# Kernel tuning notes

Hardware: AMD Instinct MI355X
Metric: run time of the kernel (lower is better)

The kernel has to match this reference:

```python
import jax, jax.numpy as jnp
import numpy as np

# model dims
D = 2048      # hidden_size
H = 16        # num_attention_heads
KV = 4        # num_key_value_heads
DH = 128      # head_dim
RD = 64       # rotary_dim (partial RoPE)
E = 8         # num_local_experts
TOPK = 2      # num_experts_per_tok
I = 1024      # intermediate_size
EPS = 1e-6
THETA = 1000000.0


def rmsnorm(h, w, eps=EPS):
    dt = h.dtype
    h32 = h.astype(jnp.float32)
    var = jnp.mean(h32 * h32, axis=-1, keepdims=True)
    return (w * (h32 * jax.lax.rsqrt(var + eps))).astype(dt)


def rotate_half(t):
    half = t.shape[-1] // 2
    return jnp.concatenate([-t[..., half:], t[..., :half]], axis=-1)


def setup_inputs() -> dict:
    key = jax.random.key(0)
    ks = jax.random.split(key, 16)
    s = lambda k, shape, sc: (jax.random.normal(k, shape, dtype=jnp.float32) * sc)
    B, S = 1, 2048
    return {
        "x": s(ks[0], (B, S, D), 1.0),
        "ln1_w": jnp.ones((D,), jnp.float32),
        "ln2_w": jnp.ones((D,), jnp.float32),
        "wq": s(ks[1], (D, H * DH), 0.02),
        "wk": s(ks[2], (D, KV * DH), 0.02),
        "wv": s(ks[3], (D, KV * DH), 0.02),
        "wo": s(ks[4], (H * DH, D), 0.02),
        "qnorm_w": jnp.ones((H * DH,), jnp.float32),
        "knorm_w": jnp.ones((KV * DH,), jnp.float32),
        "router_w": s(ks[5], (D, E), 0.02),
        "router_bias": s(ks[6], (E,), 0.1),
        "wg": s(ks[7], (E, D, I), 0.02),
        "wu": s(ks[8], (E, D, I), 0.02),
        "wd": s(ks[9], (E, I, D), 0.02),
    }


def reference(x, ln1_w, ln2_w, wq, wk, wv, wo, qnorm_w, knorm_w,
              router_w, router_bias, wg, wu, wd):
    B, S, _ = x.shape
    # ---- input RMSNorm + attention ----
    res = x
    h = rmsnorm(x, ln1_w)
    q = h @ wq                           # [B,S,H*DH]
    k = h @ wk                           # [B,S,KV*DH]
    v = h @ wv
    # MiniMax M2: QK-norm BEFORE reshape, over the full projection dim
    q = rmsnorm(q, qnorm_w)
    k = rmsnorm(k, knorm_w)
    q = q.reshape(B, S, H, DH).transpose(0, 2, 1, 3)    # [B,H,S,DH]
    k = k.reshape(B, S, KV, DH).transpose(0, 2, 1, 3)   # [B,KV,S,DH]
    v = v.reshape(B, S, KV, DH).transpose(0, 2, 1, 3)
    # partial RoPE on first RD dims of each head
    pos = jnp.arange(S, dtype=jnp.float32)
    inv_freq = 1.0 / (THETA ** (jnp.arange(0, RD, 2, dtype=jnp.float32) / RD))
    ang = pos[:, None] * inv_freq[None, :]              # [S,RD/2]
    emb = jnp.concatenate([ang, ang], axis=-1)          # [S,RD]
    cos, sin = jnp.cos(emb), jnp.sin(emb)

    def rope(t):
        rot, pas = t[..., :RD], t[..., RD:]
        rot = rot * cos + rotate_half(rot) * sin
        return jnp.concatenate([rot, pas], axis=-1)

    q, k = rope(q), rope(k)
    # GQA: repeat kv heads
    rep = H // KV
    k = jnp.repeat(k, rep, axis=1)                      # [B,H,S,DH]
    v = jnp.repeat(v, rep, axis=1)
    scores = jnp.einsum("bhqd,bhkd->bhqk", q, k) / np.sqrt(DH)
    causal = jnp.tril(jnp.ones((S, S), dtype=bool))
    scores = jnp.where(causal, scores, jnp.finfo(jnp.float32).min)
    attn = jax.nn.softmax(scores.astype(jnp.float32), axis=-1).astype(q.dtype)
    o = jnp.einsum("bhqk,bhkd->bhqd", attn, v)          # [B,H,S,DH]
    o = o.transpose(0, 2, 1, 3).reshape(B, S, H * DH) @ wo
    x1 = res + o

    # ---- post-attn RMSNorm + sigmoid-router top-k MoE ----
    h2 = rmsnorm(x1, ln2_w)
    t = h2.reshape(-1, D)                               # [T,D]
    T = t.shape[0]
    logits = t.astype(jnp.float32) @ router_w           # router in fp32
    sig = jax.nn.sigmoid(logits)                        # act before topk
    # bias only influences expert choice, not affinities
    _, topi = jax.lax.top_k(sig + router_bias, TOPK)    # [T,TOPK]
    aff = jnp.take_along_axis(sig, topi, axis=-1)
    aff = aff / jnp.sum(aff, axis=-1, keepdims=True)    # normalize_top_k_affinities
    combine = jnp.zeros((T, E), jnp.float32).at[
        jnp.arange(T)[:, None], topi].set(aff)          # [T,E] sparse combine weights
    # GLU expert MLPs (dense over experts; combine zeros out unrouted)
    gate = jnp.einsum("td,edi->tei", t, wg)
    up = jnp.einsum("td,edi->tei", t, wu)
    act = jax.nn.silu(gate) * up                        # [T,E,I]
    moe = jnp.einsum("te,tei,eid->td", combine.astype(t.dtype), act, wd)
    return x1 + moe.reshape(B, S, D)
```

## Files before the change

kernel.cpp:

```cpp
#include <hip/hip_runtime.h>
#include <hip/hip_bf16.h>
#include <stdint.h>
#include <math.h>

typedef __bf16 bf16;
typedef __bf16 bf16x8 __attribute__((ext_vector_type(8)));
typedef __bf16 bf16x4 __attribute__((ext_vector_type(4)));
typedef float  f32x4  __attribute__((ext_vector_type(4)));

#define SD 2048
#define DM 2048
#define NH 16
#define NKV 4
#define DHD 128
#define NE 8
#define NNI 1024

constexpr size_t OF_WQKVT = 0;
constexpr size_t OF_WGUT  = OF_WQKVT + 12582912ull;
constexpr size_t OF_WDT   = OF_WGUT  + 67108864ull;
constexpr size_t OF_WOT   = OF_WDT   + 33554432ull;
constexpr size_t OF_H     = OF_WOT   + 8388608ull;
constexpr size_t OF_QKV   = OF_H     + 8388608ull;
constexpr size_t OF_QB    = OF_QKV   + 25165824ull;
constexpr size_t OF_KB    = OF_QB    + 8388608ull;
constexpr size_t OF_VTB   = OF_KB    + 2097152ull;
constexpr size_t OF_X1    = OF_VTB   + 2097152ull;
constexpr size_t WS_NEED  = OF_X1    + 16777216ull;
constexpr size_t OF_ACT  = OF_QKV;
constexpr size_t OF_TB   = OF_WOT;
constexpr size_t OF_OB   = OF_H;
constexpr size_t OF_CNT  = OF_KB;
constexpr size_t OF_BLKE = OF_KB + 256;
constexpr size_t OF_BLKR = OF_KB + 512;
constexpr size_t OF_TOT  = OF_KB + 768;
constexpr size_t OF_TOPI = OF_KB + 1024;
constexpr size_t OF_TOPW = OF_KB + 16384;
constexpr size_t OF_IDXL = OF_KB + 65536;
constexpr size_t OF_WLST = OF_KB + 131072;
constexpr size_t OF_TMP0 = OF_H;
constexpr size_t OF_TMP1 = OF_WOT;

__device__ __forceinline__ void async16(void* lds, const void* g) {
  uint32_t lo = (uint32_t)(uintptr_t)lds;
  __builtin_amdgcn_global_load_lds(
      (const __attribute__((address_space(1))) uint32_t*)(uintptr_t)g,
      (__attribute__((address_space(3))) uint32_t*)lo,
      16, 0, 0);
}

__global__ void transpose_cvt(const float* __restrict__ in, int ild, long long inb,
                              bf16* __restrict__ out, int old_, long long outb,
                              int ost, int oroff)
{
  __shared__ float tile[32][33];
  const float* ip = in + (long long)blockIdx.z * inb;
  bf16* op = out + (long long)blockIdx.z * outb;
  int r0 = blockIdx.y * 32, c0 = blockIdx.x * 32;
  int tx = threadIdx.x, ty = threadIdx.y;
#pragma unroll
  for (int i = 0; i < 4; i++)
    tile[ty + i*8][tx] = ip[(size_t)(r0 + ty + i*8)*ild + c0 + tx];
  __syncthreads();
#pragma unroll
  for (int i = 0; i < 4; i++) {
    int cl = ty + i*8;
    op[(size_t)((c0 + cl)*ost + oroff)*old_ + r0 + tx] = (bf16)tile[tx][cl];
  }
}

__global__ __launch_bounds__(256)
void rmsnorm_k(const float* __restrict__ in, const float* __restrict__ w, bf16* __restrict__ outb)
{
  __shared__ float red[4];
  int s = blockIdx.x, t = threadIdx.x;
  const float* ip = in + (size_t)s * DM;
  float v[8]; float ss = 0.f;
#pragma unroll
  for (int i = 0; i < 8; i++) { v[i] = ip[t + i*256]; ss += v[i]*v[i]; }
#pragma unroll
  for (int off = 32; off > 0; off >>= 1) ss += __shfl_xor(ss, off);
  if ((t & 63) == 0) red[t >> 6] = ss;
  __syncthreads();
  float rn = rsqrtf((red[0]+red[1]+red[2]+red[3]) * (1.f/DM) + 1e-6f);
  bf16* op = outb + (size_t)s * DM;
#pragma unroll
  for (int i = 0; i < 8; i++) op[t + i*256] = (bf16)(v[i]*rn*w[t + i*256]);
}

__global__ __launch_bounds__(256)
void qrope_k(const float* __restrict__ qkv, const float* __restrict__ w, bf16* __restrict__ qout)
{
  __shared__ float row[2048];
  __shared__ float red[4];
  int s = blockIdx.x, t = threadIdx.x;
  const float* ip = qkv + (size_t)s * 3072;
  float ss = 0.f;
#pragma unroll
  for (int i = 0; i < 8; i++) { float x = ip[t + i*256]; row[t + i*256] = x; ss += x*x; }
#pragma unroll
  for (int off = 32; off > 0; off >>= 1) ss += __shfl_xor(ss, off);
  if ((t & 63) == 0) red[t >> 6] = ss;
  __syncthreads();
  float rn = rsqrtf((red[0]+red[1]+red[2]+red[3]) * (1.f/2048.f) + 1e-6f);
  const float sc = 0.08838834764831845f;
#pragma unroll
  for (int i = 0; i < 8; i++) {
    int idx = t + i*256;
    int d = idx & 127;
    float val = row[idx]*rn*w[idx];
    float o;
    if (d < 64) {
      int fi = d & 31;
      float ang = (float)s * expf(-(float)fi * (13.815510557964274f/32.f));
      float c, sn; sincosf(ang, &sn, &c);
      float pv = row[idx ^ 32]*rn*w[idx ^ 32];
      o = (d < 32) ? (val*c - pv*sn) : (val*c + pv*sn);
    } else o = val;
    qout[((size_t)(idx >> 7)*SD + s)*DHD + d] = (bf16)(o * sc);
  }
}

__global__ __launch_bounds__(128)
void krope_k(const float* __restrict__ qkv, const float* __restrict__ w, bf16* __restrict__ kout)
{
  __shared__ float row[512];
  __shared__ float red[2];
  int s = blockIdx.x, t = threadIdx.x;
  const float* ip = qkv + (size_t)s * 3072 + 2048;
  float ss = 0.f;
#pragma unroll
  for (int i = 0; i < 4; i++) { float x = ip[t + i*128]; row[t + i*128] = x; ss += x*x; }
#pragma unroll
  for (int off = 32; off > 0; off >>= 1) ss += __shfl_xor(ss, off);
  if ((t & 63) == 0) red[t >> 6] = ss;
  __syncthreads();
  float rn = rsqrtf((red[0]+red[1]) * (1.f/512.f) + 1e-6f);
#pragma unroll
  for (int i = 0; i < 4; i++) {
    int idx = t + i*128;
    int d = idx & 127;
    float val = row[idx]*rn*w[idx];
    float o;
    if (d < 64) {
      int fi = d & 31;
      float ang = (float)s * expf(-(float)fi * (13.815510557964274f/32.f));
      float c, sn; sincosf(ang, &sn, &c);
      float pv = row[idx ^ 32]*rn*w[idx ^ 32];
      o = (d < 32) ? (val*c - pv*sn) : (val*c + pv*sn);
    } else o = val;
    kout[((size_t)(idx >> 7)*SD + s)*DHD + d] = (bf16)o;
  }
}

template<int EPI>
__global__ __launch_bounds__(256)
void gemm_bt(const bf16* __restrict__ Ag, const bf16* __restrict__ Bg,
             float* __restrict__ Cg, const float* __restrict__ res,
             int M, int N, int K)
{
  __shared__ __align__(16) bf16 As[2][128*32];
  __shared__ __align__(16) bf16 Bs[2][128*32];
  const int tid = threadIdx.x;
  const int wv = tid >> 6, l = tid & 63;
  const int wm = wv >> 1, wn = wv & 1;
  const int bm = blockIdx.y * 128, bn = blockIdx.x * 128;
  const bf16* A  = Ag;
  const bf16* BT = Bg;

  f32x4 acc[4][4];
  const f32x4 vz = {0.f, 0.f, 0.f, 0.f};
#pragma unroll
  for (int i = 0; i < 4; i++)
#pragma unroll
    for (int j = 0; j < 4; j++) acc[i][j] = vz;

  auto stage = [&](int kt, int b) {
    int k0 = kt * 32;
#pragma unroll
    for (int c = 0; c < 2; c++) {
      int chunk = wv*2 + c;
      int row = chunk*16 + (l >> 2);
      int kc = (l & 3) * 8;
      async16(&As[b][chunk*512], A  + (size_t)(bm + row)*K + k0 + kc);
      async16(&Bs[b][chunk*512], BT + (size_t)(bn + row)*K + k0 + kc);
    }
  };

  int nkt = K >> 5;
  stage(0, 0);
  int buf = 0;
  for (int kt = 0; kt < nkt; ++kt) {
    __syncthreads();
    if (kt + 1 < nkt) stage(kt + 1, buf ^ 1);
    bf16x8 af[4], bfv[4];
#pragma unroll
    for (int m = 0; m < 4; m++)
      af[m] = *(const bf16x8*)&As[buf][(wm*64 + m*16 + (l & 15))*32 + (l >> 4)*8];
#pragma unroll
    for (int n = 0; n < 4; n++)
      bfv[n] = *(const bf16x8*)&Bs[buf][(wn*64 + n*16 + (l & 15))*32 + (l >> 4)*8];
#pragma unroll
    for (int m = 0; m < 4; m++)
#pragma unroll
      for (int n = 0; n < 4; n++)
        acc[m][n] = __builtin_amdgcn_mfma_f32_16x16x32_bf16(af[m], bfv[n], acc[m][n], 0, 0, 0);
    buf ^= 1;
  }

#pragma unroll
  for (int m = 0; m < 4; m++) {
#pragma unroll
    for (int n = 0; n < 4; n++) {
#pragma unroll
      for (int r = 0; r < 4; r++) {
        int row = bm + wm*64 + m*16 + (l >> 4)*4 + r;
        int col = bn + wn*64 + n*16 + (l & 15);
        float v = acc[m][n][r];
        if (EPI == 0) {
          Cg[(size_t)row*N + col] = v;
        } else {
          Cg[(size_t)row*N + col] = v + res[(size_t)row*N + col];
        }
      }
    }
  }
}

__global__ __launch_bounds__(256)
void gemm_moe_gu(const bf16* __restrict__ tb, const bf16* __restrict__ wgu,
                 bf16* __restrict__ act,
                 const int* __restrict__ cnt, const int* __restrict__ blk_e,
                 const int* __restrict__ blk_r0, const int* __restrict__ total_nblk,
                 const int* __restrict__ idxlist)
{
  const int by = blockIdx.y;
  if (by >= *total_nblk) return;
  const int e = blk_e[by], r0 = blk_r0[by], cn = cnt[e];
  __shared__ __align__(16) bf16 As[2][128*32];
  __shared__ __align__(16) bf16 Bs[2][128*32];
  const int tid = threadIdx.x;
  const int wv = tid >> 6, l = tid & 63;
  const int wm = wv >> 1, wn = wv & 1;
  const int bn = blockIdx.x * 128;
  const bf16* BT = wgu + (size_t)e*2048*2048;

  const bf16* Arow[2];
#pragma unroll
  for (int c = 0; c < 2; c++) {
    int chunk = wv*2 + c;
    int rp = r0 + chunk*16 + (l >> 2);
    int tok = (rp < cn) ? (idxlist[e*2048 + rp] & 0xFFFF) : 0;
    Arow[c] = tb + (size_t)tok*2048 + (l & 3)*8;
  }

  f32x4 acc[4][4];
  const f32x4 vz = {0.f, 0.f, 0.f, 0.f};
#pragma unroll
  for (int i = 0; i < 4; i++)
#pragma unroll
    for (int j = 0; j < 4; j++) acc[i][j] = vz;

  auto stage = [&](int kt, int b) {
    int k0 = kt * 32;
#pragma unroll
    for (int c = 0; c < 2; c++) {
      int chunk = wv*2 + c;
      int row = chunk*16 + (l >> 2);
      int kc = (l & 3) * 8;
      async16(&As[b][chunk*512], Arow[c] + k0);
      async16(&Bs[b][chunk*512], BT + (size_t)(bn + row)*2048 + k0 + kc);
    }
  };

  stage(0, 0);
  int buf = 0;
  for (int kt = 0; kt < 64; ++kt) {
    __syncthreads();
    if (kt + 1 < 64) stage(kt + 1, buf ^ 1);
    bf16x8 af[4], bfv[4];
#pragma unroll
    for (int m = 0; m < 4; m++)
      af[m] = *(const bf16x8*)&As[buf][(wm*64 + m*16 + (l & 15))*32 + (l >> 4)*8];
#pragma unroll
    for (int n = 0; n < 4; n++)
      bfv[n] = *(const bf16x8*)&Bs[buf][(wn*64 + n*16 + (l & 15))*32 + (l >> 4)*8];
#pragma unroll
    for (int m = 0; m < 4; m++)
#pragma unroll
      for (int n = 0; n < 4; n++)
        acc[m][n] = __builtin_amdgcn_mfma_f32_16x16x32_bf16(af[m], bfv[n], acc[m][n], 0, 0, 0);
    buf ^= 1;
  }

  bf16* ap = act + (size_t)e*2048*1024;
#pragma unroll
  for (int m = 0; m < 4; m++) {
#pragma unroll
    for (int n = 0; n < 4; n++) {
#pragma unroll
      for (int r = 0; r < 4; r++) {
        int lrow = wm*64 + m*16 + (l >> 4)*4 + r;
        int col = bn + wn*64 + n*16 + (l & 15);
        float v = acc[m][n][r];
        float p = __shfl_xor(v, 1);
        if (!(l & 1)) {
          float a = v / (1.f + __expf(-v)) * p;
          ap[(size_t)(r0 + lrow)*1024 + (col >> 1)] = (bf16)a;
        }
      }
    }
  }
}

__global__ __launch_bounds__(256)
void gemm_moe_dn(const bf16* __restrict__ act, const bf16* __restrict__ wdt,
                 bf16* __restrict__ tmp0, bf16* __restrict__ tmp1,
                 const int* __restrict__ cnt, const int* __restrict__ blk_e,
                 const int* __restrict__ blk_r0, const int* __restrict__ total_nblk,
                 const int* __restrict__ idxlist, const float* __restrict__ wlist)
{
  const int by = blockIdx.y;
  if (by >= *total_nblk) return;
  const int e = blk_e[by], r0 = blk_r0[by], cn = cnt[e];
  __shared__ __align__(16) bf16 As[2][128*32];
  __shared__ __align__(16) bf16 Bs[2][128*32];
  const int tid = threadIdx.x;
  const int wv = tid >> 6, l = tid & 63;
  const int wm = wv >> 1, wn = wv & 1;
  const int bn = blockIdx.x * 128;
  const bf16* A  = act + (size_t)e*2048*1024 + (size_t)r0*1024;
  const bf16* BT = wdt + (size_t)e*2048*1024;

  f32x4 acc[4][4];
  const f32x4 vz = {0.f, 0.f, 0.f, 0.f};
#pragma unroll
  for (int i = 0; i < 4; i++)
#pragma unroll
    for (int j = 0; j < 4; j++) acc[i][j] = vz;

  auto stage = [&](int kt, int b) {
    int k0 = kt * 32;
#pragma unroll
    for (int c = 0; c < 2; c++) {
      int chunk = wv*2 + c;
      int row = chunk*16 + (l >> 2);
      int kc = (l & 3) * 8;
      async16(&As[b][chunk*512], A  + (size_t)row*1024 + k0 + kc);
      async16(&Bs[b][chunk*512], BT + (size_t)(bn + row)*1024 + k0 + kc);
    }
  };

  stage(0, 0);
  int buf = 0;
  for (int kt = 0; kt < 32; ++kt) {
    __syncthreads();
    if (kt + 1 < 32) stage(kt + 1, buf ^ 1);
    bf16x8 af[4], bfv[4];
#pragma unroll
    for (int m = 0; m < 4; m++)
      af[m] = *(const bf16x8*)&As[buf][(wm*64 + m*16 + (l & 15))*32 + (l >> 4)*8];
#pragma unroll
    for (int n = 0; n < 4; n++)
      bfv[n] = *(const bf16x8*)&Bs[buf][(wn*64 + n*16 + (l & 15))*32 + (l >> 4)*8];
#pragma unroll
    for (int m = 0; m < 4; m++)
#pragma unroll
      for (int n = 0; n < 4; n++)
        acc[m][n] = __builtin_amdgcn_mfma_f32_16x16x32_bf16(af[m], bfv[n], acc[m][n], 0, 0, 0);
    buf ^= 1;
  }

#pragma unroll
  for (int m = 0; m < 4; m++) {
#pragma unroll
    for (int n = 0; n < 4; n++) {
#pragma unroll
      for (int r = 0; r < 4; r++) {
        int lrow = wm*64 + m*16 + (l >> 4)*4 + r;
        int rie = r0 + lrow;
        if (rie < cn) {
          int col = bn + wn*64 + n*16 + (l & 15);
          int pk = idxlist[e*2048 + rie];
          int t = pk & 0xFFFF, rank = pk >> 16;
          float w = wlist[e*2048 + rie];
          bf16* dst = rank ? tmp1 : tmp0;
          dst[(size_t)t*2048 + col] = (bf16)(w * acc[m][n][r]);
        }
      }
    }
  }
}

__global__ __launch_bounds__(256)
void router_k(const float* __restrict__ x1, const float* __restrict__ w2,
              const float* __restrict__ rw, const float* __restrict__ rb,
              int* __restrict__ top_i, float* __restrict__ top_w)
{
  int tok = blockIdx.x*4 + (threadIdx.x >> 6);
  int l = threadIdx.x & 63;
  const float* ip = x1 + (size_t)tok * DM;
  float tv[32]; float ss = 0.f;
#pragma unroll
  for (int i = 0; i < 32; i++) { float v = ip[l + i*64]; tv[i] = v; ss += v*v; }
#pragma unroll
  for (int off = 32; off > 0; off >>= 1) ss += __shfl_xor(ss, off);
  float rn = rsqrtf(ss * (1.f/DM) + 1e-6f);
  float acc[8];
#pragma unroll
  for (int e = 0; e < 8; e++) acc[e] = 0.f;
#pragma unroll
  for (int i = 0; i < 32; i++) {
    int d = l + i*64;
    float tval = tv[i]*rn*w2[d];
#pragma unroll
    for (int e = 0; e < 8; e++) acc[e] += tval * rw[d*8 + e];
  }
#pragma unroll
  for (int e = 0; e < 8; e++)
#pragma unroll
    for (int off = 32; off > 0; off >>= 1) acc[e] += __shfl_xor(acc[e], off);
  if (l == 0) {
    float sig[8], scv[8];
#pragma unroll
    for (int e = 0; e < 8; e++) { sig[e] = 1.f/(1.f + expf(-acc[e])); scv[e] = sig[e] + rb[e]; }
    int i0 = 0;
#pragma unroll
    for (int e = 1; e < 8; e++) if (scv[e] > scv[i0]) i0 = e;
    int i1 = (i0 == 0) ? 1 : 0;
#pragma unroll
    for (int e = 0; e < 8; e++) if (e != i0 && scv[e] > scv[i1]) i1 = e;
    float a0 = sig[i0], a1 = sig[i1], inv = 1.f/(a0 + a1);
    top_i[tok] = i0 | (i1 << 8);
    top_w[tok*2]   = a0*inv;
    top_w[tok*2+1] = a1*inv;
  }
}

__global__ __launch_bounds__(256)
void build_k(const int* __restrict__ top_i, const float* __restrict__ top_w,
             int* __restrict__ cnt, int* __restrict__ blk_e, int* __restrict__ blk_r0,
             int* __restrict__ total_nblk, int* __restrict__ idxlist, float* __restrict__ wlist)
{
  __shared__ int lcnt[8];
  int tid = threadIdx.x;
  if (tid < 8) lcnt[tid] = 0;
  __syncthreads();
  for (int t = tid; t < SD; t += 256) {
    int pk = top_i[t];
    int i0 = pk & 0xFF, i1 = (pk >> 8) & 0xFF;
    int p0 = atomicAdd(&lcnt[i0], 1);
    idxlist[i0*2048 + p0] = t;
    wlist [i0*2048 + p0] = top_w[t*2];
    int p1 = atomicAdd(&lcnt[i1], 1);
    idxlist[i1*2048 + p1] = t | (1 << 16);
    wlist [i1*2048 + p1] = top_w[t*2+1];
  }
  __syncthreads();
  if (tid < 8) cnt[tid] = lcnt[tid];
  if (tid == 0) {
    int tot = 0;
    for (int e = 0; e < 8; e++) {
      int nb = (lcnt[e] + 127) >> 7;
      for (int b = 0; b < nb; b++) { blk_e[tot] = e; blk_r0[tot] = b*128; tot++; }
    }
    *total_nblk = tot;
  }
}

__global__ __launch_bounds__(256)
void final_add(const float* __restrict__ x1, const bf16* __restrict__ t0,
               const bf16* __restrict__ t1, float* __restrict__ out)
{
  size_t i = ((size_t)blockIdx.x*256 + threadIdx.x) * 4;
  f32x4 a = *(const f32x4*)(x1 + i);
  bf16x4 b0 = *(const bf16x4*)(t0 + i);
  bf16x4 b1 = *(const bf16x4*)(t1 + i);
  f32x4 o;
#pragma unroll
  for (int j = 0; j < 4; j++) o[j] = a[j] + (float)b0[j] + (float)b1[j];
  *(f32x4*)(out + i) = o;
}

__global__ __launch_bounds__(256)
void flash(const bf16* __restrict__ qb, const bf16* __restrict__ kb,
           const bf16* __restrict__ vtb, bf16* __restrict__ ob)
{
  __shared__ __align__(16) bf16 Ks[64*128];
  __shared__ __align__(16) bf16 Vs[128*64];
  __shared__ __align__(16) bf16 Ps[4*16*64];
  const int tid = threadIdx.x, wv = tid >> 6, l = tid & 63;
  const int qt = blockIdx.x, h = blockIdx.y, g = h >> 2;

  const int qrow = qt*64 + wv*16 + (l & 15);
  bf16x8 qf[4];
#pragma unroll
  for (int f = 0; f < 4; f++)
    qf[f] = *(const bf16x8*)(qb + ((size_t)h*SD + qrow)*DHD + f*32 + (l >> 4)*8);

  float mrun[4], lrun[4];
#pragma unroll
  for (int r = 0; r < 4; r++) { mrun[r] = -1e30f; lrun[r] = 0.f; }
  f32x4 oac[8];
  const f32x4 vz = {0.f, 0.f, 0.f, 0.f};
#pragma unroll
  for (int d = 0; d < 8; d++) oac[d] = vz;

  for (int j = 0; j <= qt; ++j) {
#pragma unroll
    for (int c = 0; c < 4; c++) {
      int chunk = wv*4 + c;
      int rk = chunk*4 + (l >> 4);
      int ck = (l & 15) ^ (rk & 7);
      async16(&Ks[chunk*512], kb + ((size_t)g*SD + j*64 + rk)*DHD + ck*8);
      int rv = chunk*8 + (l >> 3);
      int cv = (l & 7) ^ (rv & 7);
      async16(&Vs[chunk*512], vtb + ((size_t)g*DHD + rv)*SD + j*64 + cv*8);
    }
    __syncthreads();

    f32x4 sf[4];
#pragma unroll
    for (int n = 0; n < 4; n++) sf[n] = vz;
#pragma unroll
    for (int f = 0; f < 4; f++) {
#pragma unroll
      for (int n = 0; n < 4; n++) {
        int row = n*16 + (l & 15);
        int cb = (f*64 + (l >> 4)*16) ^ ((row & 7) << 4);
        bf16x8 kf = *(const bf16x8*)((const char*)Ks + row*256 + cb);
        sf[n] = __builtin_amdgcn_mfma_f32_16x16x32_bf16(qf[f], kf, sf[n], 0, 0, 0);
      }
    }
    if (j == qt) {
#pragma unroll
      for (int n = 0; n < 4; n++)
#pragma unroll
        for (int r = 0; r < 4; r++) {
          int kvp = n*16 + (l & 15);
          int qp  = wv*16 + (l >> 4)*4 + r;
          if (kvp > qp) sf[n][r] = -1e30f;
        }
    }
#pragma unroll
    for (int r = 0; r < 4; r++) {
      float tm = fmaxf(fmaxf(sf[0][r], sf[1][r]), fmaxf(sf[2][r], sf[3][r]));
#pragma unroll
      for (int off = 8; off > 0; off >>= 1) tm = fmaxf(tm, __shfl_xor(tm, off));
      float mn = fmaxf(mrun[r], tm);
      float fac = __expf(mrun[r] - mn);
      mrun[r] = mn;
      float pe[4]; float ps = 0.f;
#pragma unroll
      for (int n = 0; n < 4; n++) { pe[n] = __expf(sf[n][r] - mn); ps += pe[n]; }
#pragma unroll
      for (int off = 8; off > 0; off >>= 1) ps += __shfl_xor(ps, off);
      lrun[r] = lrun[r]*fac + ps;
#pragma unroll
      for (int d = 0; d < 8; d++) oac[d][r] *= fac;
      int prow = (l >> 4)*4 + r;
#pragma unroll
      for (int n = 0; n < 4; n++) {
        int cbp = ((n*16 + (l & 15))*2) ^ ((prow & 7) << 4);
        *(bf16*)((char*)Ps + wv*2048 + prow*128 + cbp) = (bf16)pe[n];
      }
    }
#pragma unroll
    for (int ks = 0; ks < 2; ks++) {
      int pr = l & 15;
      int cbp = (ks*64 + (l >> 4)*16) ^ ((pr & 7) << 4);
      bf16x8 pa = *(const bf16x8*)((const char*)Ps + wv*2048 + pr*128 + cbp);
#pragma unroll
      for (int dt = 0; dt < 8; dt++) {
        int rv = dt*16 + (l & 15);
        int cbv = (ks*64 + (l >> 4)*16) ^ ((rv & 7) << 4);
        bf16x8 vf = *(const bf16x8*)((const char*)Vs + rv*128 + cbv);
        oac[dt] = __builtin_amdgcn_mfma_f32_16x16x32_bf16(pa, vf, oac[dt], 0, 0, 0);
      }
    }
    __syncthreads();
  }
#pragma unroll
  for (int dt = 0; dt < 8; dt++)
#pragma unroll
    for (int r = 0; r < 4; r++) {
      int s = qt*64 + wv*16 + (l >> 4)*4 + r;
      int d = dt*16 + (l & 15);
      ob[(size_t)s*DM + h*DHD + d] = (bf16)(oac[dt][r] / lrun[r]);
    }
}

extern "C" void kernel_launch(void* const* d_in, const int* in_sizes, int n_in,
                              void* d_out, int out_size, void* d_ws, size_t ws_size,
                              hipStream_t stream) {
  if (ws_size < WS_NEED) return;
  const float* x     = (const float*)d_in[0];
  const float* ln1_w = (const float*)d_in[1];
  const float* ln2_w = (const float*)d_in[2];
  const float* wq    = (const float*)d_in[3];
  const float* wk    = (const float*)d_in[4];
  const float* wv    = (const float*)d_in[5];
  const float* wo    = (const float*)d_in[6];
  const float* qnw   = (const float*)d_in[7];
  const float* knw   = (const float*)d_in[8];
  const float* rw    = (const float*)d_in[9];
  const float* rb    = (const float*)d_in[10];
  const float* wg    = (const float*)d_in[11];
  const float* wu    = (const float*)d_in[12];
  const float* wd    = (const float*)d_in[13];

  char* ws = (char*)d_ws;
  bf16*  wqkvT = (bf16*)(ws + OF_WQKVT);
  bf16*  wguT  = (bf16*)(ws + OF_WGUT);
  bf16*  wdT   = (bf16*)(ws + OF_WDT);
  bf16*  woT   = (bf16*)(ws + OF_WOT);
  bf16*  hb    = (bf16*)(ws + OF_H);
  float* qkvf  = (float*)(ws + OF_QKV);
  bf16*  qbb   = (bf16*)(ws + OF_QB);
  bf16*  kbb   = (bf16*)(ws + OF_KB);
  bf16*  vtbb  = (bf16*)(ws + OF_VTB);
  float* x1f   = (float*)(ws + OF_X1);
  bf16*  actb  = (bf16*)(ws + OF_ACT);
  bf16*  tbb   = (bf16*)(ws + OF_TB);
  bf16*  obb   = (bf16*)(ws + OF_OB);
  int*   cntp  = (int*)(ws + OF_CNT);
  int*   blke  = (int*)(ws + OF_BLKE);
  int*   blkr  = (int*)(ws + OF_BLKR);
  int*   totp  = (int*)(ws + OF_TOT);
  int*   topi  = (int*)(ws + OF_TOPI);
  float* topw  = (float*)(ws + OF_TOPW);
  int*   idxl  = (int*)(ws + OF_IDXL);
  float* wlst  = (float*)(ws + OF_WLST);
  bf16*  tmp0  = (bf16*)(ws + OF_TMP0);
  bf16*  tmp1  = (bf16*)(ws + OF_TMP1);
  float* outp  = (float*)d_out;

  dim3 b32(32, 8);
  transpose_cvt<<<dim3(64,64,1), b32, 0, stream>>>(wq, 2048, 0, wqkvT, 2048, 0, 1, 0);
  transpose_cvt<<<dim3(16,64,1), b32, 0, stream>>>(wk,  512, 0, wqkvT, 2048, 0, 1, 2048);
  transpose_cvt<<<dim3(16,64,1), b32, 0, stream>>>(wv,  512, 0, wqkvT, 2048, 0, 1, 2560);
  transpose_cvt<<<dim3(64,64,1), b32, 0, stream>>>(wo, 2048, 0, woT,   2048, 0, 1, 0);
  transpose_cvt<<<dim3(32,64,8), b32, 0, stream>>>(wg, 1024, 2048ll*1024, wguT, 2048, 2048ll*2048, 2, 0);
  transpose_cvt<<<dim3(32,64,8), b32, 0, stream>>>(wu, 1024, 2048ll*1024, wguT, 2048, 2048ll*2048, 2, 1);
  transpose_cvt<<<dim3(64,32,8), b32, 0, stream>>>(wd, 2048, 1024ll*2048, wdT,  1024, 2048ll*1024, 1, 0);

  rmsnorm_k<<<2048, 256, 0, stream>>>(x, ln1_w, hb);
  gemm_bt<0><<<dim3(24,16,1), 256, 0, stream>>>(hb, wqkvT, qkvf, nullptr, 2048, 3072, 2048);
  qrope_k<<<2048, 256, 0, stream>>>(qkvf, qnw, qbb);
  krope_k<<<2048, 128, 0, stream>>>(qkvf, knw, kbb);
  transpose_cvt<<<dim3(16,64,1), b32, 0, stream>>>(qkvf + 2560, 3072, 0, vtbb, 2048, 0, 1, 0);

  flash<<<dim3(32,16,1), 256, 0, stream>>>(qbb, kbb, vtbb, obb);

  gemm_bt<1><<<dim3(16,16,1), 256, 0, stream>>>(obb, woT, x1f, x, 2048, 2048, 2048);
  rmsnorm_k<<<2048, 256, 0, stream>>>(x1f, ln2_w, tbb);
  router_k<<<512, 256, 0, stream>>>(x1f, ln2_w, rw, rb, topi, topw);
  build_k<<<1, 256, 0, stream>>>(topi, topw, cntp, blke, blkr, totp, idxl, wlst);

  gemm_moe_gu<<<dim3(16,40,1), 256, 0, stream>>>(tbb, wguT, actb, cntp, blke, blkr, totp, idxl);
  gemm_moe_dn<<<dim3(16,40,1), 256, 0, stream>>>(actb, wdT, tmp0, tmp1, cntp, blke, blkr, totp, idxl, wlst);
  final_add<<<4096, 256, 0, stream>>>(x1f, tmp0, tmp1, outp);
}
```

Measured before the change: 630.4 us.

## Fuse prep kernels, add XCD-aware block swizzle, double-buffer flash attention

```diff
diff --git a/kernel.cpp b/kernel.cpp
--- a/kernel.cpp
+++ b/kernel.cpp
@@ -6,6 +6,7 @@
 typedef __bf16 bf16;
 typedef __bf16 bf16x8 __attribute__((ext_vector_type(8)));
 typedef __bf16 bf16x4 __attribute__((ext_vector_type(4)));
+typedef __bf16 bf16x2 __attribute__((ext_vector_type(2)));
 typedef float  f32x4  __attribute__((ext_vector_type(4)));
 
 #define SD 2048
@@ -30,11 +31,12 @@
 constexpr size_t OF_ACT  = OF_QKV;
 constexpr size_t OF_TB   = OF_WOT;
 constexpr size_t OF_OB   = OF_H;
+constexpr size_t OF_ROPET= OF_X1;
 constexpr size_t OF_CNT  = OF_KB;
-constexpr size_t OF_BLKE = OF_KB + 256;
-constexpr size_t OF_BLKR = OF_KB + 512;
-constexpr size_t OF_TOT  = OF_KB + 768;
-constexpr size_t OF_TOPI = OF_KB + 1024;
+constexpr size_t OF_BLKE = OF_KB + 512;
+constexpr size_t OF_BLKR = OF_KB + 1024;
+constexpr size_t OF_TOT  = OF_KB + 1536;
+constexpr size_t OF_TOPI = OF_KB + 2048;
 constexpr size_t OF_TOPW = OF_KB + 16384;
 constexpr size_t OF_IDXL = OF_KB + 65536;
 constexpr size_t OF_WLST = OF_KB + 131072;
@@ -49,124 +51,164 @@
       16, 0, 0);
 }
 
-__global__ void transpose_cvt(const float* __restrict__ in, int ild, long long inb,
-                              bf16* __restrict__ out, int old_, long long outb,
-                              int ost, int oroff)
-{
-  __shared__ float tile[32][33];
-  const float* ip = in + (long long)blockIdx.z * inb;
-  bf16* op = out + (long long)blockIdx.z * outb;
-  int r0 = blockIdx.y * 32, c0 = blockIdx.x * 32;
-  int tx = threadIdx.x, ty = threadIdx.y;
+__device__ __forceinline__ void tr32(const float* __restrict__ ip, int ild,
+                                     bf16* __restrict__ op, int old_, int ost, int oroff,
+                                     int r0, int c0, int t, float* sm)
+{
+  int tx = t & 31, ty = t >> 5;
 #pragma unroll
   for (int i = 0; i < 4; i++)
-    tile[ty + i*8][tx] = ip[(size_t)(r0 + ty + i*8)*ild + c0 + tx];
+    sm[(ty + i*8)*33 + tx] = ip[(size_t)(r0 + ty + i*8)*ild + c0 + tx];
   __syncthreads();
 #pragma unroll
-  for (int i = 0; i < 4; i++) {
-    int cl = ty + i*8;
-    op[(size_t)((c0 + cl)*ost + oroff)*old_ + r0 + tx] = (bf16)tile[tx][cl];
-  }
-}
-
-__global__ __launch_bounds__(256)
-void rmsnorm_k(const float* __restrict__ in, const float* __restrict__ w, bf16* __restrict__ outb)
-{
-  __shared__ float red[4];
-  int s = blockIdx.x, t = threadIdx.x;
-  const float* ip = in + (size_t)s * DM;
-  float v[8]; float ss = 0.f;
-#pragma unroll
-  for (int i = 0; i < 8; i++) { v[i] = ip[t + i*256]; ss += v[i]*v[i]; }
-#pragma unroll
-  for (int off = 32; off > 0; off >>= 1) ss += __shfl_xor(ss, off);
-  if ((t & 63) == 0) red[t >> 6] = ss;
-  __syncthreads();
-  float rn = rsqrtf((red[0]+red[1]+red[2]+red[3]) * (1.f/DM) + 1e-6f);
-  bf16* op = outb + (size_t)s * DM;
-#pragma unroll
-  for (int i = 0; i < 8; i++) op[t + i*256] = (bf16)(v[i]*rn*w[t + i*256]);
-}
-
-__global__ __launch_bounds__(256)
-void qrope_k(const float* __restrict__ qkv, const float* __restrict__ w, bf16* __restrict__ qout)
-{
-  __shared__ float row[2048];
-  __shared__ float red[4];
-  int s = blockIdx.x, t = threadIdx.x;
-  const float* ip = qkv + (size_t)s * 3072;
-  float ss = 0.f;
-#pragma unroll
-  for (int i = 0; i < 8; i++) { float x = ip[t + i*256]; row[t + i*256] = x; ss += x*x; }
-#pragma unroll
-  for (int off = 32; off > 0; off >>= 1) ss += __shfl_xor(ss, off);
-  if ((t & 63) == 0) red[t >> 6] = ss;
-  __syncthreads();
-  float rn = rsqrtf((red[0]+red[1]+red[2]+red[3]) * (1.f/2048.f) + 1e-6f);
-  const float sc = 0.08838834764831845f;
-#pragma unroll
-  for (int i = 0; i < 8; i++) {
-    int idx = t + i*256;
-    int d = idx & 127;
-    float val = row[idx]*rn*w[idx];
-    float o;
-    if (d < 64) {
-      int fi = d & 31;
-      float ang = (float)s * expf(-(float)fi * (13.815510557964274f/32.f));
-      float c, sn; sincosf(ang, &sn, &c);
-      float pv = row[idx ^ 32]*rn*w[idx ^ 32];
-      o = (d < 32) ? (val*c - pv*sn) : (val*c + pv*sn);
-    } else o = val;
-    qout[((size_t)(idx >> 7)*SD + s)*DHD + d] = (bf16)(o * sc);
-  }
-}
-
-__global__ __launch_bounds__(128)
-void krope_k(const float* __restrict__ qkv, const float* __restrict__ w, bf16* __restrict__ kout)
-{
-  __shared__ float row[512];
-  __shared__ float red[2];
-  int s = blockIdx.x, t = threadIdx.x;
-  const float* ip = qkv + (size_t)s * 3072 + 2048;
-  float ss = 0.f;
-#pragma unroll
-  for (int i = 0; i < 4; i++) { float x = ip[t + i*128]; row[t + i*128] = x; ss += x*x; }
-#pragma unroll
-  for (int off = 32; off > 0; off >>= 1) ss += __shfl_xor(ss, off);
-  if ((t & 63) == 0) red[t >> 6] = ss;
-  __syncthreads();
-  float rn = rsqrtf((red[0]+red[1]) * (1.f/512.f) + 1e-6f);
-#pragma unroll
-  for (int i = 0; i < 4; i++) {
-    int idx = t + i*128;
-    int d = idx & 127;
-    float val = row[idx]*rn*w[idx];
-    float o;
-    if (d < 64) {
-      int fi = d & 31;
-      float ang = (float)s * expf(-(float)fi * (13.815510557964274f/32.f));
-      float c, sn; sincosf(ang, &sn, &c);
-      float pv = row[idx ^ 32]*rn*w[idx ^ 32];
-      o = (d < 32) ? (val*c - pv*sn) : (val*c + pv*sn);
-    } else o = val;
-    kout[((size_t)(idx >> 7)*SD + s)*DHD + d] = (bf16)o;
+  for (int k = 0; k < 2; k++) {
+    int p = t + k*256;
+    int cl = p >> 4, rp = (p & 15)*2;
+    bf16x2 pk = { (bf16)sm[rp*33 + cl], (bf16)sm[(rp+1)*33 + cl] };
+    *(bf16x2*)&op[(size_t)((c0 + cl)*ost + oroff)*old_ + r0 + rp] = pk;
+  }
+}
+
+__global__ __launch_bounds__(256)
+void prep_k(const float* __restrict__ x, const float* __restrict__ ln1w,
+            const float* __restrict__ wq, const float* __restrict__ wk,
+            const float* __restrict__ wvv, const float* __restrict__ wo,
+            const float* __restrict__ wg, const float* __restrict__ wu,
+            const float* __restrict__ wd,
+            float* __restrict__ ropet, bf16* __restrict__ hb,
+            bf16* __restrict__ wqkvT, bf16* __restrict__ woT,
+            bf16* __restrict__ wguT, bf16* __restrict__ wdT)
+{
+  __shared__ float smem[1056];
+  int bid = blockIdx.x, t = threadIdx.x;
+  if (bid < 2048) {
+    int s = bid;
+    const float* ip = x + (size_t)s * DM;
+    float v[8]; float ss = 0.f;
+#pragma unroll
+    for (int i = 0; i < 8; i++) { v[i] = ip[t + i*256]; ss += v[i]*v[i]; }
+#pragma unroll
+    for (int off = 32; off > 0; off >>= 1) ss += __shfl_xor(ss, off);
+    if ((t & 63) == 0) smem[t >> 6] = ss;
+    __syncthreads();
+    float rn = rsqrtf((smem[0]+smem[1]+smem[2]+smem[3]) * (1.f/DM) + 1e-6f);
+    bf16* op = hb + (size_t)s * DM;
+#pragma unroll
+    for (int i = 0; i < 8; i++) op[t + i*256] = (bf16)(v[i]*rn*ln1w[t + i*256]);
+  } else if (bid < 2304) {
+    int i = (bid - 2048)*256 + t;
+    int s = i >> 5, fi = i & 31;
+    float ang = (float)s * expf(-(float)fi * (13.815510557964274f/32.f));
+    float c, sn; sincosf(ang, &sn, &c);
+    ropet[i*2]   = c;
+    ropet[i*2+1] = sn;
+  } else if (bid < 6400) {
+    int j = bid - 2304;
+    tr32(wq, 2048, wqkvT, 2048, 1, 0, (j>>6)*32, (j&63)*32, t, smem);
+  } else if (bid < 7424) {
+    int j = bid - 6400;
+    tr32(wk, 512, wqkvT, 2048, 1, 2048, (j>>4)*32, (j&15)*32, t, smem);
+  } else if (bid < 8448) {
+    int j = bid - 7424;
+    tr32(wvv, 512, wqkvT, 2048, 1, 2560, (j>>4)*32, (j&15)*32, t, smem);
+  } else if (bid < 12544) {
+    int j = bid - 8448;
+    tr32(wo, 2048, woT, 2048, 1, 0, (j>>6)*32, (j&63)*32, t, smem);
+  } else if (bid < 28928) {
+    int j = bid - 12544; int e = j >> 11, r = j & 2047;
+    tr32(wg + (size_t)e*2048*1024, 1024, wguT + (size_t)e*2048*2048, 2048, 2, 0,
+         (r>>5)*32, (r&31)*32, t, smem);
+  } else if (bid < 45312) {
+    int j = bid - 28928; int e = j >> 11, r = j & 2047;
+    tr32(wu + (size_t)e*2048*1024, 1024, wguT + (size_t)e*2048*2048, 2048, 2, 1,
+         (r>>5)*32, (r&31)*32, t, smem);
+  } else {
+    int j = bid - 45312; int e = j >> 11, r = j & 2047;
+    tr32(wd + (size_t)e*1024*2048, 2048, wdT + (size_t)e*2048*1024, 1024, 1, 0,
+         (r>>6)*32, (r&63)*32, t, smem);
+  }
+}
+
+__global__ __launch_bounds__(256)
+void qkv_post_k(const float* __restrict__ qkvf, const float* __restrict__ qnw,
+                const float* __restrict__ knw, const float* __restrict__ ropet,
+                bf16* __restrict__ qbb, bf16* __restrict__ kbb, bf16* __restrict__ vtbb)
+{
+  __shared__ float smem[2052];
+  int bid = blockIdx.x, t = threadIdx.x;
+  const float2* tab2 = (const float2*)ropet;
+  if (bid < 2048) {
+    int s = bid;
+    const float* ip = qkvf + (size_t)s * 3072;
+    float* row = smem; float* red = smem + 2048;
+    float ss = 0.f;
+#pragma unroll
+    for (int i = 0; i < 8; i++) { float v = ip[t + i*256]; row[t + i*256] = v; ss += v*v; }
+#pragma unroll
+    for (int off = 32; off > 0; off >>= 1) ss += __shfl_xor(ss, off);
+    if ((t & 63) == 0) red[t >> 6] = ss;
+    __syncthreads();
+    float rn = rsqrtf((red[0]+red[1]+red[2]+red[3]) * (1.f/2048.f) + 1e-6f);
+    const float sc = 0.08838834764831845f;
+#pragma unroll
+    for (int i = 0; i < 8; i++) {
+      int idx = t + i*256;
+      int d = idx & 127;
+      float val = row[idx]*rn*qnw[idx];
+      float o;
+      if (d < 64) {
+        float2 cs = tab2[s*32 + (d & 31)];
+        float pv = row[idx ^ 32]*rn*qnw[idx ^ 32];
+        o = (d < 32) ? (val*cs.x - pv*cs.y) : (val*cs.x + pv*cs.y);
+      } else o = val;
+      qbb[((size_t)(idx >> 7)*SD + s)*DHD + d] = (bf16)(o * sc);
+    }
+  } else if (bid < 4096) {
+    int s = bid - 2048;
+    const float* ip = qkvf + (size_t)s * 3072 + 2048;
+    float* row = smem; float* red = smem + 512;
+    float v0 = ip[t], v1 = ip[t + 256];
+    row[t] = v0; row[t + 256] = v1;
+    float ss = v0*v0 + v1*v1;
+#pragma unroll
+    for (int off = 32; off > 0; off >>= 1) ss += __shfl_xor(ss, off);
+    if ((t & 63) == 0) red[t >> 6] = ss;
+    __syncthreads();
+    float rn = rsqrtf((red[0]+red[1]+red[2]+red[3]) * (1.f/512.f) + 1e-6f);
+#pragma unroll
+    for (int i = 0; i < 2; i++) {
+      int idx = t + i*256;
+      int d = idx & 127;
+      float val = row[idx]*rn*knw[idx];
+      float o;
+      if (d < 64) {
+        float2 cs = tab2[s*32 + (d & 31)];
+        float pv = row[idx ^ 32]*rn*knw[idx ^ 32];
+        o = (d < 32) ? (val*cs.x - pv*cs.y) : (val*cs.x + pv*cs.y);
+      } else o = val;
+      kbb[((size_t)(idx >> 7)*SD + s)*DHD + d] = (bf16)o;
+    }
+  } else {
+    int j = bid - 4096;
+    tr32(qkvf + 2560, 3072, vtbb, 2048, 1, 0, (j>>4)*32, (j&15)*32, t, smem);
   }
 }
 
 template<int EPI>
 __global__ __launch_bounds__(256)
-void gemm_bt(const bf16* __restrict__ Ag, const bf16* __restrict__ Bg,
+void gemm_bt(const bf16* __restrict__ A, const bf16* __restrict__ BT,
              float* __restrict__ Cg, const float* __restrict__ res,
-             int M, int N, int K)
+             int N, int K, int nbm)
 {
   __shared__ __align__(16) bf16 As[2][128*32];
   __shared__ __align__(16) bf16 Bs[2][128*32];
+  const int nwg = gridDim.x, cpx = nwg >> 3;
+  const int id = blockIdx.x;
+  const int swz = (id & 7)*cpx + (id >> 3);
+  const int bm = (swz % nbm)*128, bn = (swz / nbm)*128;
   const int tid = threadIdx.x;
   const int wv = tid >> 6, l = tid & 63;
   const int wm = wv >> 1, wn = wv & 1;
-  const int bm = blockIdx.y * 128, bn = blockIdx.x * 128;
-  const bf16* A  = Ag;
-  const bf16* BT = Bg;
 
   f32x4 acc[4][4];
   const f32x4 vz = {0.f, 0.f, 0.f, 0.f};
@@ -177,11 +219,11 @@
 
   auto stage = [&](int kt, int b) {
     int k0 = kt * 32;
+    int kc = (l & 3) * 8;
 #pragma unroll
     for (int c = 0; c < 2; c++) {
       int chunk = wv*2 + c;
       int row = chunk*16 + (l >> 2);
-      int kc = (l & 3) * 8;
       async16(&As[b][chunk*512], A  + (size_t)(bm + row)*K + k0 + kc);
       async16(&Bs[b][chunk*512], BT + (size_t)(bn + row)*K + k0 + kc);
     }
@@ -217,11 +259,8 @@
         int row = bm + wm*64 + m*16 + (l >> 4)*4 + r;
         int col = bn + wn*64 + n*16 + (l & 15);
         float v = acc[m][n][r];
-        if (EPI == 0) {
-          Cg[(size_t)row*N + col] = v;
-        } else {
-          Cg[(size_t)row*N + col] = v + res[(size_t)row*N + col];
-        }
+        if (EPI == 0) Cg[(size_t)row*N + col] = v;
+        else          Cg[(size_t)row*N + col] = v + res[(size_t)row*N + col];
       }
     }
   }
@@ -234,7 +273,11 @@
                  const int* __restrict__ blk_r0, const int* __restrict__ total_nblk,
                  const int* __restrict__ idxlist)
 {
-  const int by = blockIdx.y;
+  const int nwg = gridDim.x, cpx = nwg >> 3;
+  const int id = blockIdx.x;
+  const int swz = (id & 7)*cpx + (id >> 3);
+  const int bn = (swz / 40)*128;
+  const int by = swz % 40;
   if (by >= *total_nblk) return;
   const int e = blk_e[by], r0 = blk_r0[by], cn = cnt[e];
   __shared__ __align__(16) bf16 As[2][128*32];
@@ -242,7 +285,6 @@
   const int tid = threadIdx.x;
   const int wv = tid >> 6, l = tid & 63;
   const int wm = wv >> 1, wn = wv & 1;
-  const int bn = blockIdx.x * 128;
   const bf16* BT = wgu + (size_t)e*2048*2048;
 
   const bf16* Arow[2];
@@ -263,11 +305,11 @@
 
   auto stage = [&](int kt, int b) {
     int k0 = kt * 32;
+    int kc = (l & 3) * 8;
 #pragma unroll
     for (int c = 0; c < 2; c++) {
       int chunk = wv*2 + c;
       int row = chunk*16 + (l >> 2);
-      int kc = (l & 3) * 8;
       async16(&As[b][chunk*512], Arow[c] + k0);
       async16(&Bs[b][chunk*512], BT + (size_t)(bn + row)*2048 + k0 + kc);
     }
@@ -320,7 +362,11 @@
                  const int* __restrict__ blk_r0, const int* __restrict__ total_nblk,
                  const int* __restrict__ idxlist, const float* __restrict__ wlist)
 {
-  const int by = blockIdx.y;
+  const int nwg = gridDim.x, cpx = nwg >> 3;
+  const int id = blockIdx.x;
+  const int swz = (id & 7)*cpx + (id >> 3);
+  const int bn = (swz / 40)*128;
+  const int by = swz % 40;
   if (by >= *total_nblk) return;
   const int e = blk_e[by], r0 = blk_r0[by], cn = cnt[e];
   __shared__ __align__(16) bf16 As[2][128*32];
@@ -328,7 +374,6 @@
   const int tid = threadIdx.x;
   const int wv = tid >> 6, l = tid & 63;
   const int wm = wv >> 1, wn = wv & 1;
-  const int bn = blockIdx.x * 128;
   const bf16* A  = act + (size_t)e*2048*1024 + (size_t)r0*1024;
   const bf16* BT = wdt + (size_t)e*2048*1024;
 
@@ -341,11 +386,11 @@
 
   auto stage = [&](int kt, int b) {
     int k0 = kt * 32;
+    int kc = (l & 3) * 8;
 #pragma unroll
     for (int c = 0; c < 2; c++) {
       int chunk = wv*2 + c;
       int row = chunk*16 + (l >> 2);
-      int kc = (l & 3) * 8;
       async16(&As[b][chunk*512], A  + (size_t)row*1024 + k0 + kc);
       async16(&Bs[b][chunk*512], BT + (size_t)(bn + row)*1024 + k0 + kc);
     }
@@ -382,14 +427,33 @@
         if (rie < cn) {
           int col = bn + wn*64 + n*16 + (l & 15);
           int pk = idxlist[e*2048 + rie];
-          int t = pk & 0xFFFF, rank = pk >> 16;
+          int tkn = pk & 0xFFFF, rank = pk >> 16;
           float w = wlist[e*2048 + rie];
           bf16* dst = rank ? tmp1 : tmp0;
-          dst[(size_t)t*2048 + col] = (bf16)(w * acc[m][n][r]);
+          dst[(size_t)tkn*2048 + col] = (bf16)(w * acc[m][n][r]);
         }
       }
     }
   }
+}
+
+__global__ __launch_bounds__(256)
+void rmsnorm_k(const float* __restrict__ in, const float* __restrict__ w, bf16* __restrict__ outb)
+{
+  __shared__ float red[4];
+  int s = blockIdx.x, t = threadIdx.x;
+  const float* ip = in + (size_t)s * DM;
+  float v[8]; float ss = 0.f;
+#pragma unroll
+  for (int i = 0; i < 8; i++) { v[i] = ip[t + i*256]; ss += v[i]*v[i]; }
+#pragma unroll
+  for (int off = 32; off > 0; off >>= 1) ss += __shfl_xor(ss, off);
+  if ((t & 63) == 0) red[t >> 6] = ss;
+  __syncthreads();
+  float rn = rsqrtf((red[0]+red[1]+red[2]+red[3]) * (1.f/DM) + 1e-6f);
+  bf16* op = outb + (size_t)s * DM;
+#pragma unroll
+  for (int i = 0; i < 8; i++) op[t + i*256] = (bf16)(v[i]*rn*w[t + i*256]);
 }
 
 __global__ __launch_bounds__(256)
@@ -486,11 +550,12 @@
 void flash(const bf16* __restrict__ qb, const bf16* __restrict__ kb,
            const bf16* __restrict__ vtb, bf16* __restrict__ ob)
 {
-  __shared__ __align__(16) bf16 Ks[64*128];
-  __shared__ __align__(16) bf16 Vs[128*64];
+  __shared__ __align__(16) bf16 Ks[2][64*128];
+  __shared__ __align__(16) bf16 Vs[2][128*64];
   __shared__ __align__(16) bf16 Ps[4*16*64];
   const int tid = threadIdx.x, wv = tid >> 6, l = tid & 63;
-  const int qt = blockIdx.x, h = blockIdx.y, g = h >> 2;
+  const int h = blockIdx.y, g = h >> 2;
+  const int qt = (h & 8) ? (31 - (int)blockIdx.x) : (int)blockIdx.x;
 
   const int qrow = qt*64 + wv*16 + (l & 15);
   bf16x8 qf[4];
@@ -506,32 +571,40 @@
 #pragma unroll
   for (int d = 0; d < 8; d++) oac[d] = vz;
 
-  for (int j = 0; j <= qt; ++j) {
+  auto stage = [&](int j, int b) {
 #pragma unroll
     for (int c = 0; c < 4; c++) {
       int chunk = wv*4 + c;
       int rk = chunk*4 + (l >> 4);
       int ck = (l & 15) ^ (rk & 7);
-      async16(&Ks[chunk*512], kb + ((size_t)g*SD + j*64 + rk)*DHD + ck*8);
+      async16(&Ks[b][chunk*512], kb + ((size_t)g*SD + j*64 + rk)*DHD + ck*8);
       int rv = chunk*8 + (l >> 3);
       int cv = (l & 7) ^ (rv & 7);
-      async16(&Vs[chunk*512], vtb + ((size_t)g*DHD + rv)*SD + j*64 + cv*8);
-    }
+      async16(&Vs[b][chunk*512], vtb + ((size_t)g*DHD + rv)*SD + j*64 + cv*8);
+    }
+  };
+
+  stage(0, 0);
+  int buf = 0;
+  for (int j = 0; j <= qt; ++j) {
     __syncthreads();
+    if (j < qt) stage(j + 1, buf ^ 1);
 
     f32x4 sf[4];
 #pragma unroll
     for (int n = 0; n < 4; n++) sf[n] = vz;
+    __builtin_amdgcn_s_setprio(1);
 #pragma unroll
     for (int f = 0; f < 4; f++) {
 #pragma unroll
       for (int n = 0; n < 4; n++) {
         int row = n*16 + (l & 15);
         int cb = (f*64 + (l >> 4)*16) ^ ((row & 7) << 4);
-        bf16x8 kf = *(const bf16x8*)((const char*)Ks + row*256 + cb);
+        bf16x8 kf = *(const bf16x8*)((const char*)Ks[buf] + row*256 + cb);
         sf[n] = __builtin_amdgcn_mfma_f32_16x16x32_bf16(qf[f], kf, sf[n], 0, 0, 0);
       }
     }
+    __builtin_amdgcn_s_setprio(0);
     if (j == qt) {
 #pragma unroll
       for (int n = 0; n < 4; n++)
@@ -565,6 +638,7 @@
         *(bf16*)((char*)Ps + wv*2048 + prow*128 + cbp) = (bf16)pe[n];
       }
     }
+    __builtin_amdgcn_s_setprio(1);
 #pragma unroll
     for (int ks = 0; ks < 2; ks++) {
       int pr = l & 15;
@@ -574,11 +648,12 @@
       for (int dt = 0; dt < 8; dt++) {
         int rv = dt*16 + (l & 15);
         int cbv = (ks*64 + (l >> 4)*16) ^ ((rv & 7) << 4);
-        bf16x8 vf = *(const bf16x8*)((const char*)Vs + rv*128 + cbv);
+        bf16x8 vf = *(const bf16x8*)((const char*)Vs[buf] + rv*128 + cbv);
         oac[dt] = __builtin_amdgcn_mfma_f32_16x16x32_bf16(pa, vf, oac[dt], 0, 0, 0);
       }
     }
-    __syncthreads();
+    __builtin_amdgcn_s_setprio(0);
+    buf ^= 1;
   }
 #pragma unroll
   for (int dt = 0; dt < 8; dt++)
@@ -620,6 +695,7 @@
   bf16*  kbb   = (bf16*)(ws + OF_KB);
   bf16*  vtbb  = (bf16*)(ws + OF_VTB);
   float* x1f   = (float*)(ws + OF_X1);
+  float* ropet = (float*)(ws + OF_ROPET);
   bf16*  actb  = (bf16*)(ws + OF_ACT);
   bf16*  tbb   = (bf16*)(ws + OF_TB);
   bf16*  obb   = (bf16*)(ws + OF_OB);
@@ -635,29 +711,16 @@
   bf16*  tmp1  = (bf16*)(ws + OF_TMP1);
   float* outp  = (float*)d_out;
 
-  dim3 b32(32, 8);
-  transpose_cvt<<<dim3(64,64,1), b32, 0, stream>>>(wq, 2048, 0, wqkvT, 2048, 0, 1, 0);
-  transpose_cvt<<<dim3(16,64,1), b32, 0, stream>>>(wk,  512, 0, wqkvT, 2048, 0, 1, 2048);
-  transpose_cvt<<<dim3(16,64,1), b32, 0, stream>>>(wv,  512, 0, wqkvT, 2048, 0, 1, 2560);
-  transpose_cvt<<<dim3(64,64,1), b32, 0, stream>>>(wo, 2048, 0, woT,   2048, 0, 1, 0);
-  transpose_cvt<<<dim3(32,64,8), b32, 0, stream>>>(wg, 1024, 2048ll*1024, wguT, 2048, 2048ll*2048, 2, 0);
-  transpose_cvt<<<dim3(32,64,8), b32, 0, stream>>>(wu, 1024, 2048ll*1024, wguT, 2048, 2048ll*2048, 2, 1);
-  transpose_cvt<<<dim3(64,32,8), b32, 0, stream>>>(wd, 2048, 1024ll*2048, wdT,  1024, 2048ll*1024, 1, 0);
-
-  rmsnorm_k<<<2048, 256, 0, stream>>>(x, ln1_w, hb);
-  gemm_bt<0><<<dim3(24,16,1), 256, 0, stream>>>(hb, wqkvT, qkvf, nullptr, 2048, 3072, 2048);
-  qrope_k<<<2048, 256, 0, stream>>>(qkvf, qnw, qbb);
-  krope_k<<<2048, 128, 0, stream>>>(qkvf, knw, kbb);
-  transpose_cvt<<<dim3(16,64,1), b32, 0, stream>>>(qkvf + 2560, 3072, 0, vtbb, 2048, 0, 1, 0);
-
+  prep_k<<<61696, 256, 0, stream>>>(x, ln1_w, wq, wk, wv, wo, wg, wu, wd,
+                                    ropet, hb, wqkvT, woT, wguT, wdT);
+  gemm_bt<0><<<384, 256, 0, stream>>>(hb, wqkvT, qkvf, nullptr, 3072, 2048, 16);
+  qkv_post_k<<<5120, 256, 0, stream>>>(qkvf, qnw, knw, ropet, qbb, kbb, vtbb);
   flash<<<dim3(32,16,1), 256, 0, stream>>>(qbb, kbb, vtbb, obb);
-
-  gemm_bt<1><<<dim3(16,16,1), 256, 0, stream>>>(obb, woT, x1f, x, 2048, 2048, 2048);
+  gemm_bt<1><<<256, 256, 0, stream>>>(obb, woT, x1f, x, 2048, 2048, 16);
   rmsnorm_k<<<2048, 256, 0, stream>>>(x1f, ln2_w, tbb);
   router_k<<<512, 256, 0, stream>>>(x1f, ln2_w, rw, rb, topi, topw);
   build_k<<<1, 256, 0, stream>>>(topi, topw, cntp, blke, blkr, totp, idxl, wlst);
-
-  gemm_moe_gu<<<dim3(16,40,1), 256, 0, stream>>>(tbb, wguT, actb, cntp, blke, blkr, totp, idxl);
-  gemm_moe_dn<<<dim3(16,40,1), 256, 0, stream>>>(actb, wdT, tmp0, tmp1, cntp, blke, blkr, totp, idxl, wlst);
+  gemm_moe_gu<<<640, 256, 0, stream>>>(tbb, wguT, actb, cntp, blke, blkr, totp, idxl);
+  gemm_moe_dn<<<640, 256, 0, stream>>>(actb, wdT, tmp0, tmp1, cntp, blke, blkr, totp, idxl, wlst);
   final_add<<<4096, 256, 0, stream>>>(x1f, tmp0, tmp1, outp);
 }
```

Result: faster. 593.9 us (-5.8%).
